# Performance work log

Measured on AMD Instinct MI355X. Metric: run time of the kernel, lower is better.

Reference implementation:

```python
import jax, jax.numpy as jnp
import numpy as np

N = 65536      # total nodes
B = 512        # graphs (equal-sized)
NPER = N // B  # 128 nodes per graph
E = 655360     # edges
F_IN = 128
K = 32         # sort-pool k
OUT = 27


def _gcn(x, row, col, dinv, W, b):
    # PyG GCNConv with added self-loops and symmetric normalization:
    xw = x @ W                                   # [N, F_out]
    coef = dinv[row] * dinv[col]                 # [E]
    agg = jax.ops.segment_sum(xw[row] * coef[:, None], col, num_segments=N)
    return agg + (dinv * dinv)[:, None] * xw + b  # self-loop term + bias


def _conv1d(x, w, b, stride):
    # x: [B, C_in, L], w: [C_out, C_in, K]
    out = jax.lax.conv_general_dilated(x, w, (stride,), 'VALID',
                                       dimension_numbers=('NCH', 'OIH', 'NCH'))
    return out + b[None, :, None]


def setup_inputs() -> dict:
    key = jax.random.key(0)
    ks = jax.random.split(key, 16)
    x = jax.random.normal(ks[0], (N, F_IN), dtype=jnp.float32)
    edge_index = jax.random.randint(ks[1], (2, E), 0, N, dtype=jnp.int32)
    batch = jnp.repeat(jnp.arange(B, dtype=jnp.int32), NPER)

    def lin(k, fi, fo):
        return jax.random.normal(k, (fi, fo), dtype=jnp.float32) / np.sqrt(fi)

    W1, b1 = lin(ks[2], F_IN, 128), jnp.zeros((128,), jnp.float32)
    W2, b2 = lin(ks[3], 128, 64), jnp.zeros((64,), jnp.float32)
    W3, b3 = lin(ks[4], 64, 32), jnp.zeros((32,), jnp.float32)
    W4, b4 = lin(ks[5], 32, 32), jnp.zeros((32,), jnp.float32)
    conv5_w = jax.random.normal(ks[6], (16, 1, 256), jnp.float32) / np.sqrt(256)
    conv5_b = jnp.zeros((16,), jnp.float32)
    conv6_w = jax.random.normal(ks[7], (32, 16, 5), jnp.float32) / np.sqrt(16 * 5)
    conv6_b = jnp.zeros((32,), jnp.float32)
    dense_w = lin(ks[8], 384, OUT)
    dense_b = jnp.zeros((OUT,), jnp.float32)
    return dict(x=x, edge_index=edge_index, batch=batch,
                W1=W1, b1=b1, W2=W2, b2=b2, W3=W3, b3=b3, W4=W4, b4=b4,
                conv5_w=conv5_w, conv5_b=conv5_b, conv6_w=conv6_w, conv6_b=conv6_b,
                dense_w=dense_w, dense_b=dense_b)


def reference(x, edge_index, batch, W1, b1, W2, b2, W3, b3, W4, b4,
              conv5_w, conv5_b, conv6_w, conv6_b, dense_w, dense_b):
    row, col = edge_index[0], edge_index[1]
    deg = jax.ops.segment_sum(jnp.ones((E,), x.dtype), col, num_segments=N) + 1.0
    dinv = jax.lax.rsqrt(deg)

    x1 = jnp.tanh(_gcn(x, row, col, dinv, W1, b1))
    x2 = jnp.tanh(_gcn(x1, row, col, dinv, W2, b2))
    x3 = jnp.tanh(_gcn(x2, row, col, dinv, W3, b3))
    x4 = jnp.tanh(_gcn(x3, row, col, dinv, W4, b4))
    h = jnp.concatenate([x1, x2, x3, x4], axis=-1)   # [N, 256]

    # SortAggregation: sort nodes within each graph by last channel (desc), take top-k.
    hg = h.reshape(B, NPER, 256)
    idx = jnp.argsort(-hg[:, :, -1], axis=1)[:, :K]                 # [B, K]
    pooled = jnp.take_along_axis(hg, idx[:, :, None], axis=1)       # [B, K, 256]
    top_k_indices = idx + (jnp.arange(B, dtype=idx.dtype) * NPER)[:, None]

    z = pooled.reshape(B, 1, K * 256)                # [B, 1, 8192]
    z = jax.nn.relu(_conv1d(z, conv5_w, conv5_b, 256))  # [B, 16, 32]
    z = jax.lax.reduce_window(z, -jnp.inf, jax.lax.max,
                              (1, 1, 2), (1, 1, 2), 'VALID')        # [B, 16, 16]
    z = jax.nn.relu(_conv1d(z, conv6_w, conv6_b, 1))  # [B, 32, 12]
    z = z.reshape(B, -1)                              # [B, 384]
    out = z @ dense_w + dense_b                       # [B, 27]
    return out, top_k_indices
```

## Files before the change

kernel.cpp:

```cpp
#include <hip/hip_runtime.h>
#include <math.h>

#define N_NODES 65536
#define N_EDGES 655360
#define N_GRAPHS 512
#define NPERG 128
#define KTOP 32
#define NOUT 27
#define OUT0_SIZE (N_GRAPHS * NOUT)
#define EPS 64

typedef unsigned int uint32;
typedef unsigned short u16;
typedef unsigned char u8;
typedef __attribute__((ext_vector_type(8))) short bf16x8;
typedef __attribute__((ext_vector_type(4))) float f32x4;
typedef __attribute__((ext_vector_type(2))) float f32x2;

__device__ __forceinline__ float blo(uint32 u) { return __uint_as_float(u << 16); }
__device__ __forceinline__ float bhi(uint32 u) { return __uint_as_float(u & 0xffff0000u); }
__device__ __forceinline__ u16 f2b(float f) {
    uint32 u = __float_as_uint(f);
    u += 0x7fffu + ((u >> 16) & 1u);
    return (u16)(u >> 16);
}
__device__ __forceinline__ uint32 pk(float a, float b) {
    return (uint32)f2b(a) | ((uint32)f2b(b) << 16);
}
__device__ __forceinline__ f32x2 fp8lo(uint32 u) { return __builtin_amdgcn_cvt_pk_f32_fp8((int)u, false); }
__device__ __forceinline__ f32x2 fp8hi(uint32 u) { return __builtin_amdgcn_cvt_pk_f32_fp8((int)u, true); }
__device__ __forceinline__ u8 f2fp8(float v) {
    return (u8)(__builtin_amdgcn_cvt_pk_fp8_f32(v, v, 0, false) & 0xff);
}


template<int FI, int FO>
__device__ __forceinline__ void pack_w(const float* __restrict__ W, uint4* __restrict__ pw,
                                       int base, int nb) {
    constexpr int KC = FI / 8;
    for (int q = (blockIdx.x - base) * 256 + threadIdx.x; q < FO * KC; q += nb * 256) {
        int n = q % FO, c = q / FO;
        const float* wp = W + (size_t)(c * 8) * FO + n;
        uint4 v;
        v.x = pk(wp[0],            wp[(size_t)FO]);
        v.y = pk(wp[2*(size_t)FO], wp[3*(size_t)FO]);
        v.z = pk(wp[4*(size_t)FO], wp[5*(size_t)FO]);
        v.w = pk(wp[6*(size_t)FO], wp[7*(size_t)FO]);
        pw[n * KC + c] = v;
    }
}

__global__ __launch_bounds__(256) void prep_kernel(const float* __restrict__ W1, const float* __restrict__ W2,
                                                   const float* __restrict__ W3, const float* __restrict__ W4,
                                                   uint4* __restrict__ pw1, uint4* __restrict__ pw2,
                                                   uint4* __restrict__ pw3, uint4* __restrict__ pw4,
                                                   int* __restrict__ cur) {
    int b = blockIdx.x;
    if (b < 256) { cur[b * 256 + threadIdx.x] = 0; return; }
    b -= 256;
    if (b < 8)       pack_w<128, 128>(W1, pw1, 256, 8);
    else if (b < 12) pack_w<128, 64>(W2, pw2, 264, 4);
    else if (b < 13) pack_w<64, 32>(W3, pw3, 268, 1);
    else             pack_w<32, 32>(W4, pw4, 269, 1);
}


__global__ __launch_bounds__(256) void fill_kernel(const int* __restrict__ erow, const int* __restrict__ ecol,
                                                   int* __restrict__ cur, u16* __restrict__ ep) {
    int e = blockIdx.x * 256 + threadIdx.x;
    int r = erow[e], d = ecol[e];
    int slot = atomicAdd(&cur[d], 1);
    if (slot < EPS) ep[(d << 6) + slot] = (u16)r;
}


template<int FI, int FO>
__device__ __forceinline__ void stage_Bp(const uint4* __restrict__ pw, uint4* __restrict__ Bs) {
    constexpr int KC = FI / 8, SA = KC + 1;
    for (int q = threadIdx.x; q < FO * KC; q += 256) {
        int n = q / KC, c = q % KC;
        Bs[n * SA + c] = pw[q];
    }
}

template<int FI, int FO, bool OUT_FP8>
__device__ __forceinline__ void mfma_store(uint4* __restrict__ As, const uint4* __restrict__ Bs,
                                           uint4* __restrict__ Y, size_t rowbase,
                                           const float* __restrict__ ds) {
    constexpr int KC = FI / 8, SA = KC + 1;
    constexpr int NTILE = FO / 16;
    constexpr int CW = (NTILE >= 4) ? 4 : NTILE;
    constexpr int NTW = NTILE / CW;
    constexpr int RW = 4 / CW;
    constexpr int RS = 2 / RW;
    constexpr int KSTEPS = FI / 32;
    int t = threadIdx.x;
    int w = t >> 6, L = t & 63;
    int quad = L >> 4, m = L & 15;
    int cw = w % CW, rw = w / CW;

    const bf16x8* Asv = (const bf16x8*)As;
    const bf16x8* Bsv = (const bf16x8*)Bs;

    f32x4 acc[RS][NTW];
#pragma unroll
    for (int i = 0; i < RS; i++)
#pragma unroll
        for (int j = 0; j < NTW; j++) acc[i][j] = (f32x4)0.f;

#pragma unroll
    for (int ks = 0; ks < KSTEPS; ks++) {
        int kc = ks * 4 + quad;
        bf16x8 bfr[NTW];
#pragma unroll
        for (int j = 0; j < NTW; j++) {
            int n = (cw * NTW + j) * 16 + m;
            bfr[j] = Bsv[n * SA + kc];
        }
#pragma unroll
        for (int i = 0; i < RS; i++) {
            int r = (rw * RS + i) * 16 + m;
            bf16x8 afr = Asv[r * SA + kc];
#pragma unroll
            for (int j = 0; j < NTW; j++)
                acc[i][j] = __builtin_amdgcn_mfma_f32_16x16x32_bf16(afr, bfr[j], acc[i][j], 0, 0, 0);
        }
    }
    __syncthreads();

    if constexpr (OUT_FP8) {
        u8* outs = (u8*)As;
#pragma unroll
        for (int i = 0; i < RS; i++) {
            int rb = (rw * RS + i) * 16 + quad * 4;
#pragma unroll
            for (int j = 0; j < NTW; j++) {
                int cc = (cw * NTW + j) * 16 + m;
#pragma unroll
                for (int g2 = 0; g2 < 4; g2++)
                    outs[(rb + g2) * FO + cc] = f2fp8(acc[i][j][g2] * ds[rb + g2]);
            }
        }
    } else {
        u16* outs = (u16*)As;
#pragma unroll
        for (int i = 0; i < RS; i++) {
            int rb = (rw * RS + i) * 16 + quad * 4;
#pragma unroll
            for (int j = 0; j < NTW; j++) {
                int cc = (cw * NTW + j) * 16 + m;
#pragma unroll
                for (int g2 = 0; g2 < 4; g2++)
                    outs[(rb + g2) * FO + cc] = f2b(acc[i][j][g2] * ds[rb + g2]);
            }
        }
    }
    __syncthreads();
    constexpr int NU4 = OUT_FP8 ? (32 * FO / 16) : (32 * FO / 8);
    for (int q = t; q < NU4; q += 256)
        Y[rowbase * (NU4 / 32) + q] = ((const uint4*)As)[q];
}


__global__ __launch_bounds__(256) void gemm1_kernel(const float* __restrict__ x,
                                                    const uint4* __restrict__ pw1,
                                                    const int* __restrict__ cur,
                                                    uint4* __restrict__ xw1) {
    constexpr int KC = 16, SA = 17;
    __shared__ __align__(16) uint4 As[32 * SA];
    __shared__ __align__(16) uint4 Bs[128 * SA];
    __shared__ float ds[32];
    int t = threadIdx.x;
    stage_Bp<128, 128>(pw1, Bs);
    size_t rowbase = (size_t)blockIdx.x * 32;
    if (t < 32) ds[t] = rsqrtf((float)cur[rowbase + t] + 1.0f);
    for (int q = t; q < 32 * KC; q += 256) {
        int r = q / KC, c = q % KC;
        const float* xp = x + (rowbase + r) * 128 + c * 8;
        float4 v0 = *(const float4*)xp;
        float4 v1 = *(const float4*)(xp + 4);
        uint4 u;
        u.x = pk(v0.x, v0.y); u.y = pk(v0.z, v0.w);
        u.z = pk(v1.x, v1.y); u.w = pk(v1.z, v1.w);
        As[r * SA + c] = u;
    }
    __syncthreads();
    mfma_store<128, 128, true>(As, Bs, xw1, rowbase, ds);
}


template<int F>
__device__ __forceinline__ void gath8_fp8v(const uint2* __restrict__ x2, uint4 e8,
                                           int cl, int rem, float (&ac)[8]) {
    constexpr int LN = F / 8;
    uint32 qq[8] = { e8.x & 0xffffu, e8.x >> 16, e8.y & 0xffffu, e8.y >> 16,
                     e8.z & 0xffffu, e8.z >> 16, e8.w & 0xffffu, e8.w >> 16 };
#pragma unroll
    for (int j = 0; j < 8; j++) {
        bool ok = j < rem;
        uint32 src = ok ? qq[j] : 0u;
        uint2 g = x2[(size_t)src * LN + cl];
        uint32 gx = ok ? g.x : 0u, gy = ok ? g.y : 0u;
        f32x2 l0 = fp8lo(gx), h0 = fp8hi(gx), l1 = fp8lo(gy), h1 = fp8hi(gy);
        ac[0] += l0.x; ac[1] += l0.y; ac[2] += h0.x; ac[3] += h0.y;
        ac[4] += l1.x; ac[5] += l1.y; ac[6] += h1.x; ac[7] += h1.y;
    }
}

template<int F>
__device__ __forceinline__ void agg_node_fp8v(const uint2* __restrict__ x2,
                                              const u16* __restrict__ ep,
                                              int n, int cl, int deg, float dn,
                                              const float* __restrict__ bias, float (&r)[8]) {
    constexpr int LN = F / 8;
    const u16* epp = ep + (n << 6);
    float ac[8];
#pragma unroll
    for (int c = 0; c < 8; c++) ac[c] = 0.f;
    uint4 e0 = *(const uint4*)(epp);
    uint4 e1 = *(const uint4*)(epp + 8);
    gath8_fp8v<F>(x2, e0, cl, deg, ac);
    gath8_fp8v<F>(x2, e1, cl, deg - 8, ac);
    if (deg > 16) {
        int nb = min((deg + 7) >> 3, EPS / 8);
        for (int b = 2; b < nb; b++) {
            uint4 e8 = *(const uint4*)(epp + b * 8);
            gath8_fp8v<F>(x2, e8, cl, deg - b * 8, ac);
        }
    }
    uint2 sv = x2[(size_t)n * LN + cl];
    f32x2 l0 = fp8lo(sv.x), h0 = fp8hi(sv.x), l1 = fp8lo(sv.y), h1 = fp8hi(sv.y);
    float sf[8] = { l0.x, l0.y, h0.x, h0.y, l1.x, l1.y, h1.x, h1.y };
#pragma unroll
    for (int c = 0; c < 8; c++) r[c] = dn * (ac[c] + sf[c]) + bias[8 * cl + c];
}


template<int F, int FO, bool OUT_FP8>
__global__ __launch_bounds__(256, 6) void agg_gemm8(const uint2* __restrict__ xin,
                                                    const int* __restrict__ cur,
                                                    const u16* __restrict__ ep,
                                                    const float* __restrict__ bias,
                                                    const uint4* __restrict__ pw,
                                                    uint4* __restrict__ hc4, int co4,
                                                    uint4* __restrict__ xout) {
    constexpr int KC = F / 8, SA = KC + 1;
    constexpr int LN = F / 8;
    constexpr int NPP = 256 / LN;
    __shared__ __align__(16) uint4 As[32 * SA];
    __shared__ __align__(16) uint4 Bs[FO * SA];
    __shared__ float ds[32];
    int t = threadIdx.x;
    int rowbase = blockIdx.x * 32;
    stage_Bp<F, FO>(pw, Bs);
    if (t < 32) ds[t] = rsqrtf((float)cur[rowbase + t] + 1.0f);
    __syncthreads();

    int cl = t % LN, nsub = t / LN;
#pragma unroll
    for (int pass = 0; pass < 32 / NPP; pass++) {
        int nl = pass * NPP + nsub;
        int n = rowbase + nl;
        int deg = cur[n];
        float r[8];
        agg_node_fp8v<F>(xin, ep, n, cl, deg, ds[nl], bias, r);
        uint4 pr;
        pr.x = pk(tanhf(r[0]), tanhf(r[1]));
        pr.y = pk(tanhf(r[2]), tanhf(r[3]));
        pr.z = pk(tanhf(r[4]), tanhf(r[5]));
        pr.w = pk(tanhf(r[6]), tanhf(r[7]));
        hc4[(size_t)n * 32 + co4 + cl] = pr;
        As[nl * SA + cl] = pr;
    }
    __syncthreads();
    mfma_store<F, FO, OUT_FP8>(As, Bs, xout, (size_t)rowbase, ds);
}


template<int L4>
__device__ __forceinline__ void gath8_bf16(const uint2* __restrict__ x2, uint4 e8,
                                           int c4, int rem, float (&ac)[4][4]) {
    uint32 qq[8] = { e8.x & 0xffffu, e8.x >> 16, e8.y & 0xffffu, e8.y >> 16,
                     e8.z & 0xffffu, e8.z >> 16, e8.w & 0xffffu, e8.w >> 16 };
#pragma unroll
    for (int j = 0; j < 8; j++) {
        bool ok = j < rem;
        uint32 src = ok ? qq[j] : 0u;
        uint2 g = x2[(size_t)src * L4 + c4];
        uint32 gx = ok ? g.x : 0u, gy = ok ? g.y : 0u;
        ac[j & 3][0] += blo(gx); ac[j & 3][1] += bhi(gx);
        ac[j & 3][2] += blo(gy); ac[j & 3][3] += bhi(gy);
    }
}

template<int F>
__device__ __forceinline__ void agg_node_bf16(const uint2* __restrict__ x2,
                                              const u16* __restrict__ ep,
                                              int n, int c4, int deg, float dn,
                                              const float* __restrict__ bias,
                                              float& r0, float& r1, float& r2, float& r3) {
    constexpr int L4 = F / 4;
    const u16* epp = ep + (n << 6);
    float ac[4][4];
#pragma unroll
    for (int i = 0; i < 4; i++)
#pragma unroll
        for (int j = 0; j < 4; j++) ac[i][j] = 0.f;
    uint4 e0 = *(const uint4*)(epp);
    uint4 e1 = *(const uint4*)(epp + 8);
    gath8_bf16<L4>(x2, e0, c4, deg, ac);
    gath8_bf16<L4>(x2, e1, c4, deg - 8, ac);
    if (deg > 16) {
        int nb = min((deg + 7) >> 3, EPS / 8);
        for (int b = 2; b < nb; b++) {
            uint4 e8 = *(const uint4*)(epp + b * 8);
            gath8_bf16<L4>(x2, e8, c4, deg - b * 8, ac);
        }
    }
    float s0 = (ac[0][0] + ac[1][0]) + (ac[2][0] + ac[3][0]);
    float s1 = (ac[0][1] + ac[1][1]) + (ac[2][1] + ac[3][1]);
    float s2 = (ac[0][2] + ac[1][2]) + (ac[2][2] + ac[3][2]);
    float s3 = (ac[0][3] + ac[1][3]) + (ac[2][3] + ac[3][3]);
    uint2 sv = x2[(size_t)n * L4 + c4];
    r0 = dn * (s0 + blo(sv.x)) + bias[4 * c4 + 0];
    r1 = dn * (s1 + bhi(sv.x)) + bias[4 * c4 + 1];
    r2 = dn * (s2 + blo(sv.y)) + bias[4 * c4 + 2];
    r3 = dn * (s3 + bhi(sv.y)) + bias[4 * c4 + 3];
}


template<int F, int FO>
__global__ __launch_bounds__(256, 6) void agg_gemm_bf(const uint32* __restrict__ xin,
                                                      const int* __restrict__ cur,
                                                      const u16* __restrict__ ep,
                                                      const float* __restrict__ bias,
                                                      const uint4* __restrict__ pw,
                                                      uint32* __restrict__ hc, int co2,
                                                      uint4* __restrict__ xout) {
    constexpr int KC = F / 8, SA = KC + 1;
    constexpr int L4 = F / 4;
    constexpr int NPP = 256 / L4;
    __shared__ __align__(16) uint4 As[32 * SA];
    __shared__ __align__(16) uint4 Bs[FO * SA];
    __shared__ float ds[32];
    int t = threadIdx.x;
    int rowbase = blockIdx.x * 32;
    stage_Bp<F, FO>(pw, Bs);
    if (t < 32) ds[t] = rsqrtf((float)cur[rowbase + t] + 1.0f);
    __syncthreads();

    uint2* As2 = (uint2*)As;
    uint2* hc2 = (uint2*)hc;
    int c4 = t % L4;
    int nsub = t / L4;
#pragma unroll
    for (int pass = 0; pass < 32 / NPP; pass++) {
        int nl = pass * NPP + nsub;
        int n = rowbase + nl;
        int deg = cur[n];
        float r0, r1, r2, r3;
        agg_node_bf16<F>((const uint2*)xin, ep, n, c4, deg, ds[nl], bias, r0, r1, r2, r3);
        uint2 pr;
        pr.x = pk(tanhf(r0), tanhf(r1));
        pr.y = pk(tanhf(r2), tanhf(r3));
        hc2[(size_t)n * 64 + co2 + c4] = pr;
        As2[nl * (SA * 2) + c4] = pr;
    }
    __syncthreads();
    mfma_store<F, FO, false>(As, Bs, xout, (size_t)rowbase, ds);
}


__device__ __forceinline__ void key_g8(const uint32* __restrict__ xw, uint4 e8,
                                       int rem, float (&ac3)[4]) {
    uint32 qq[8] = { e8.x & 0xffffu, e8.x >> 16, e8.y & 0xffffu, e8.y >> 16,
                     e8.z & 0xffffu, e8.z >> 16, e8.w & 0xffffu, e8.w >> 16 };
#pragma unroll
    for (int j = 0; j < 8; j++) {
        bool ok = j < rem;
        uint32 src = ok ? qq[j] : 0u;
        uint32 gy = xw[(size_t)src * 16 + 15];
        ac3[j & 3] += bhi(ok ? gy : 0u);
    }
}

__global__ __launch_bounds__(256) void final_kernel(const uint32* __restrict__ hc,
                                                    const uint32* __restrict__ xw4,
                                                    const int* __restrict__ cur,
                                                    const u16* __restrict__ ep,
                                                    const float* __restrict__ b4,
                                                    const float* __restrict__ w5, const float* __restrict__ b5,
                                                    const float* __restrict__ w6, const float* __restrict__ b6,
                                                    const float* __restrict__ dw, const float* __restrict__ db,
                                                    float* __restrict__ out) {
    __shared__ float skey[128];
    __shared__ int   sidx[128];
    __shared__ uint32 ph[32 * 133];
    __shared__ __align__(16) float w5s[4096];
    __shared__ float z5[16 * 33];
    __shared__ float ms[16 * 17];
    __shared__ float z6[384];
    int g = blockIdx.x, t = threadIdx.x;

    if (t >= 128) {
        for (int q = t - 128; q < 1024; q += 128)
            ((float4*)w5s)[q] = ((const float4*)w5)[q];
    } else {
        int n = g * NPERG + t;
        int deg = cur[n];
        float dn = rsqrtf((float)deg + 1.0f);
        const u16* epp = ep + (n << 6);
        float ac3[4] = { 0.f, 0.f, 0.f, 0.f };
        uint4 e0 = *(const uint4*)(epp);
        uint4 e1 = *(const uint4*)(epp + 8);
        key_g8(xw4, e0, deg, ac3);
        key_g8(xw4, e1, deg - 8, ac3);
        if (deg > 16) {
            int nb = min((deg + 7) >> 3, EPS / 8);
            for (int b = 2; b < nb; b++) {
                uint4 e8 = *(const uint4*)(epp + b * 8);
                key_g8(xw4, e8, deg - b * 8, ac3);
            }
        }
        float s3 = (ac3[0] + ac3[1]) + (ac3[2] + ac3[3]);
        uint32 svy = xw4[(size_t)n * 16 + 15];
        float r3 = dn * (s3 + bhi(svy)) + b4[31];
        skey[t] = __uint_as_float(((uint32)f2b(tanhf(r3))) << 16);
        sidx[t] = t;
    }
    __syncthreads();

    for (int sz = 2; sz <= 128; sz <<= 1) {
        for (int stride = sz >> 1; stride > 0; stride >>= 1) {
            if (t < 64) {
                int i = ((t & ~(stride - 1)) << 1) | (t & (stride - 1));
                int j = i | stride;
                float ki = skey[i], kj = skey[j];
                int ii = sidx[i], ij = sidx[j];
                bool desc = ((i & sz) == 0);
                bool ibef = (ki > kj) || (ki == kj && ii < ij);
                if (desc != ibef) { skey[i] = kj; skey[j] = ki; sidx[i] = ij; sidx[j] = ii; }
            }
            __syncthreads();
        }
    }

    if (t < KTOP) out[OUT0_SIZE + g * KTOP + t] = (float)(g * NPERG + sidx[t]);

    {
        int r = t >> 3, c4 = t & 7;
        int n = g * NPERG + sidx[r];
        int deg = cur[n];
        float dn = rsqrtf((float)deg + 1.0f);
        float r0, r1, r2, r3;
        agg_node_bf16<32>((const uint2*)xw4, ep, n, c4, deg, dn, b4, r0, r1, r2, r3);
        uint32* dst = &ph[r * 133 + 112 + 2 * c4];
        dst[0] = pk(tanhf(r0), tanhf(r1));
        dst[1] = pk(tanhf(r2), tanhf(r3));
    }

    {
        const uint4* hcv = (const uint4*)hc;
        for (int q = t; q < 1024; q += 256) {
            int cell = q & 31;
            if (cell >= 28) continue;
            int r2 = q >> 5;
            int node = g * NPERG + sidx[r2];
            uint4 v = hcv[(size_t)node * 32 + cell];
            uint32* dst = &ph[r2 * 133 + cell * 4];
            dst[0] = v.x; dst[1] = v.y; dst[2] = v.z; dst[3] = v.w;
        }
    }
    __syncthreads();

    {
        int o = t >> 5, l = t & 31;
        float a0 = 0.f, a1 = 0.f;
#pragma unroll 4
        for (int j2 = 0; j2 < 128; j2++) {
            uint32 u = ph[l * 133 + j2];
            float p0 = blo(u), p1 = bhi(u);
            a0 += p0 * w5s[o * 256 + 2 * j2]       + p1 * w5s[o * 256 + 2 * j2 + 1];
            a1 += p0 * w5s[(o + 8) * 256 + 2 * j2] + p1 * w5s[(o + 8) * 256 + 2 * j2 + 1];
        }
        z5[o * 33 + l]       = fmaxf(a0 + b5[o], 0.f);
        z5[(o + 8) * 33 + l] = fmaxf(a1 + b5[o + 8], 0.f);
    }
    __syncthreads();

    {
        int o = t >> 4, p = t & 15;
        ms[o * 17 + p] = fmaxf(z5[o * 33 + 2 * p], z5[o * 33 + 2 * p + 1]);
    }
    __syncthreads();

    for (int q = t; q < 384; q += 256) {
        int o2 = q / 12, tt = q % 12;
        float a = b6[o2];
        for (int o = 0; o < 16; o++) {
#pragma unroll
            for (int k = 0; k < 5; k++)
                a += w6[(o2 * 16 + o) * 5 + k] * ms[o * 17 + tt + k];
        }
        z6[q] = fmaxf(a, 0.f);
    }
    __syncthreads();

    if (t < NOUT) {
        float a = db[t];
        for (int i = 0; i < 384; i++) a += z6[i] * dw[i * NOUT + t];
        out[g * NOUT + t] = a;
    }
}


extern "C" void kernel_launch(void* const* d_in, const int* in_sizes, int n_in,
                              void* d_out, int out_size, void* d_ws, size_t ws_size,
                              hipStream_t stream) {
    const float* x    = (const float*)d_in[0];
    const int*   edge = (const int*)d_in[1];
    const int*   erow = edge;
    const int*   ecol = edge + N_EDGES;
    const float* W1 = (const float*)d_in[3];  const float* b1 = (const float*)d_in[4];
    const float* W2 = (const float*)d_in[5];  const float* b2 = (const float*)d_in[6];
    const float* W3 = (const float*)d_in[7];  const float* b3 = (const float*)d_in[8];
    const float* W4 = (const float*)d_in[9];  const float* b4 = (const float*)d_in[10];
    const float* w5 = (const float*)d_in[11]; const float* b5 = (const float*)d_in[12];
    const float* w6 = (const float*)d_in[13]; const float* b6 = (const float*)d_in[14];
    const float* dw = (const float*)d_in[15]; const float* db = (const float*)d_in[16];
    float* out = (float*)d_out;

    char* wsb = (char*)d_ws;
    size_t off = 0;
    auto alloc = [&](size_t bytes) -> void* {
        void* p = wsb + off;
        off = (off + bytes + 255) & ~(size_t)255;
        return p;
    };
    int*    cur  = (int*)   alloc((size_t)N_NODES * 4);
    u16*    ep   = (u16*)   alloc((size_t)N_NODES * EPS * 2);
    uint32* xwA  = (uint32*)alloc((size_t)N_NODES * 32 * 4);
    uint32* xwB  = (uint32*)alloc((size_t)N_NODES * 32 * 4);
    uint32* hc   = (uint32*)alloc((size_t)N_NODES * 128 * 4);
    uint4*  pw1  = (uint4*) alloc(2048 * 16);
    uint4*  pw2  = (uint4*) alloc(1024 * 16);
    uint4*  pw3  = (uint4*) alloc(256 * 16);
    uint4*  pw4  = (uint4*) alloc(128 * 16);
    (void)ws_size; (void)in_sizes; (void)n_in; (void)out_size;

    prep_kernel<<<270, 256, 0, stream>>>(W1, W2, W3, W4, pw1, pw2, pw3, pw4, cur);
    fill_kernel<<<N_EDGES / 256, 256, 0, stream>>>(erow, ecol, cur, ep);
    gemm1_kernel<<<N_NODES / 32, 256, 0, stream>>>(x, pw1, cur, (uint4*)xwA);
    agg_gemm8<128, 64, true><<<N_NODES / 32, 256, 0, stream>>>((const uint2*)xwA, cur, ep, b1, pw2, (uint4*)hc, 0, (uint4*)xwB);
    agg_gemm8<64, 32, false><<<N_NODES / 32, 256, 0, stream>>>((const uint2*)xwB, cur, ep, b2, pw3, (uint4*)hc, 16, (uint4*)xwA);
    agg_gemm_bf<32, 32><<<N_NODES / 32, 256, 0, stream>>>(xwA, cur, ep, b3, pw4, hc, 48, (uint4*)xwB);
    final_kernel<<<N_GRAPHS, 256, 0, stream>>>(hc, xwB, cur, ep, b4, w5, b5, w6, b6, dw, db, out);
}
```

Before: 226.1 us.

## Widen layer-1 gathers, batch first 16 neighbor loads, add nontemporal stores

Adds a new agg_gemm16 kernel for layer 1 in which each thread gathers 16 fp8 channels (uint4) per neighbor and handles one node, instead of 8 channels over several passes. The fp8 and bf16 aggregation helpers now issue all 16 neighbor loads before accumulating, to raise memory-level parallelism. Edge index and x reads and the concatenated-feature stores switch to nontemporal loads and stores to limit cache pollution. The changes cost more registers per thread, which could lower occupancy.

```diff
diff --git a/kernel.cpp b/kernel.cpp
--- a/kernel.cpp
+++ b/kernel.cpp
@@ -16,6 +16,9 @@
 typedef __attribute__((ext_vector_type(8))) short bf16x8;
 typedef __attribute__((ext_vector_type(4))) float f32x4;
 typedef __attribute__((ext_vector_type(2))) float f32x2;
+typedef __attribute__((ext_vector_type(4))) float f32x4n;
+typedef __attribute__((ext_vector_type(4))) uint32 u32x4;
+typedef __attribute__((ext_vector_type(2))) uint32 u32x2;
 
 __device__ __forceinline__ float blo(uint32 u) { return __uint_as_float(u << 16); }
 __device__ __forceinline__ float bhi(uint32 u) { return __uint_as_float(u & 0xffff0000u); }
@@ -31,6 +34,15 @@
 __device__ __forceinline__ f32x2 fp8hi(uint32 u) { return __builtin_amdgcn_cvt_pk_f32_fp8((int)u, true); }
 __device__ __forceinline__ u8 f2fp8(float v) {
     return (u8)(__builtin_amdgcn_cvt_pk_fp8_f32(v, v, 0, false) & 0xff);
+}
+
+__device__ __forceinline__ void nts4(uint4* p, uint4 v) {
+    u32x4 vv; vv.x = v.x; vv.y = v.y; vv.z = v.z; vv.w = v.w;
+    __builtin_nontemporal_store(vv, (u32x4*)p);
+}
+__device__ __forceinline__ void nts2(uint2* p, uint2 v) {
+    u32x2 vv; vv.x = v.x; vv.y = v.y;
+    __builtin_nontemporal_store(vv, (u32x2*)p);
 }
 
 
@@ -68,7 +80,8 @@
 __global__ __launch_bounds__(256) void fill_kernel(const int* __restrict__ erow, const int* __restrict__ ecol,
                                                    int* __restrict__ cur, u16* __restrict__ ep) {
     int e = blockIdx.x * 256 + threadIdx.x;
-    int r = erow[e], d = ecol[e];
+    int r = __builtin_nontemporal_load(erow + e);
+    int d = __builtin_nontemporal_load(ecol + e);
     int slot = atomicAdd(&cur[d], 1);
     if (slot < EPS) ep[(d << 6) + slot] = (u16)r;
 }
@@ -176,9 +189,9 @@
     if (t < 32) ds[t] = rsqrtf((float)cur[rowbase + t] + 1.0f);
     for (int q = t; q < 32 * KC; q += 256) {
         int r = q / KC, c = q % KC;
-        const float* xp = x + (rowbase + r) * 128 + c * 8;
-        float4 v0 = *(const float4*)xp;
-        float4 v1 = *(const float4*)(xp + 4);
+        const f32x4n* xp4 = (const f32x4n*)(x + (rowbase + r) * 128 + c * 8);
+        f32x4n v0 = __builtin_nontemporal_load(xp4);
+        f32x4n v1 = __builtin_nontemporal_load(xp4 + 1);
         uint4 u;
         u.x = pk(v0.x, v0.y); u.y = pk(v0.z, v0.w);
         u.z = pk(v1.x, v1.y); u.w = pk(v1.z, v1.w);
@@ -186,6 +199,96 @@
     }
     __syncthreads();
     mfma_store<128, 128, true>(As, Bs, xw1, rowbase, ds);
+}
+
+
+__device__ __forceinline__ void gath8_fp8w(const uint4* __restrict__ x4, uint4 e8,
+                                           int cl, int rem, float (&ac)[16]) {
+    uint32 qq[8] = { e8.x & 0xffffu, e8.x >> 16, e8.y & 0xffffu, e8.y >> 16,
+                     e8.z & 0xffffu, e8.z >> 16, e8.w & 0xffffu, e8.w >> 16 };
+#pragma unroll
+    for (int j = 0; j < 8; j++) {
+        bool ok = j < rem;
+        uint32 src = ok ? qq[j] : 0u;
+        uint4 g = x4[(size_t)src * 8 + cl];
+        uint32 gw0 = ok ? g.x : 0u, gw1 = ok ? g.y : 0u;
+        uint32 gw2 = ok ? g.z : 0u, gw3 = ok ? g.w : 0u;
+        f32x2 a0 = fp8lo(gw0), b0 = fp8hi(gw0), a1 = fp8lo(gw1), b1 = fp8hi(gw1);
+        f32x2 a2 = fp8lo(gw2), b2 = fp8hi(gw2), a3 = fp8lo(gw3), b3 = fp8hi(gw3);
+        ac[0] += a0.x;  ac[1] += a0.y;  ac[2] += b0.x;  ac[3] += b0.y;
+        ac[4] += a1.x;  ac[5] += a1.y;  ac[6] += b1.x;  ac[7] += b1.y;
+        ac[8] += a2.x;  ac[9] += a2.y;  ac[10] += b2.x; ac[11] += b2.y;
+        ac[12] += a3.x; ac[13] += a3.y; ac[14] += b3.x; ac[15] += b3.y;
+    }
+}
+
+__device__ __forceinline__ void agg_node_fp8w(const uint4* __restrict__ x4,
+                                              const u16* __restrict__ ep,
+                                              int n, int cl, int deg, float dn,
+                                              const float* __restrict__ bias, float (&r)[16]) {
+    const u16* epp = ep + (n << 6);
+    float ac[16];
+#pragma unroll
+    for (int c = 0; c < 16; c++) ac[c] = 0.f;
+    uint4 e0 = *(const uint4*)(epp);
+    uint4 e1 = *(const uint4*)(epp + 8);
+    gath8_fp8w(x4, e0, cl, deg, ac);
+    gath8_fp8w(x4, e1, cl, deg - 8, ac);
+    if (deg > 16) {
+        int nb = min((deg + 7) >> 3, EPS / 8);
+        for (int b = 2; b < nb; b++) {
+            uint4 e8 = *(const uint4*)(epp + b * 8);
+            gath8_fp8w(x4, e8, cl, deg - b * 8, ac);
+        }
+    }
+    uint4 sv = x4[(size_t)n * 8 + cl];
+    f32x2 a0 = fp8lo(sv.x), b0 = fp8hi(sv.x), a1 = fp8lo(sv.y), b1 = fp8hi(sv.y);
+    f32x2 a2 = fp8lo(sv.z), b2 = fp8hi(sv.z), a3 = fp8lo(sv.w), b3 = fp8hi(sv.w);
+    float sf[16] = { a0.x, a0.y, b0.x, b0.y, a1.x, a1.y, b1.x, b1.y,
+                     a2.x, a2.y, b2.x, b2.y, a3.x, a3.y, b3.x, b3.y };
+#pragma unroll
+    for (int c = 0; c < 16; c++) r[c] = dn * (ac[c] + sf[c]) + bias[16 * cl + c];
+}
+
+
+template<int FO>
+__global__ __launch_bounds__(256, 6) void agg_gemm16(const uint4* __restrict__ xin,
+                                                     const int* __restrict__ cur,
+                                                     const u16* __restrict__ ep,
+                                                     const float* __restrict__ bias,
+                                                     const uint4* __restrict__ pw,
+                                                     uint4* __restrict__ hc4, int co4,
+                                                     uint4* __restrict__ xout) {
+    constexpr int KC = 16, SA = 17;
+    __shared__ __align__(16) uint4 As[32 * SA];
+    __shared__ __align__(16) uint4 Bs[FO * SA];
+    __shared__ float ds[32];
+    int t = threadIdx.x;
+    int rowbase = blockIdx.x * 32;
+    stage_Bp<128, FO>(pw, Bs);
+    if (t < 32) ds[t] = rsqrtf((float)cur[rowbase + t] + 1.0f);
+    __syncthreads();
+
+    int cl = t & 7, nl = t >> 3;
+    int n = rowbase + nl;
+    int deg = cur[n];
+    float r[16];
+    agg_node_fp8w(xin, ep, n, cl, deg, ds[nl], bias, r);
+    uint4 pr0, pr1;
+    pr0.x = pk(tanhf(r[0]),  tanhf(r[1]));
+    pr0.y = pk(tanhf(r[2]),  tanhf(r[3]));
+    pr0.z = pk(tanhf(r[4]),  tanhf(r[5]));
+    pr0.w = pk(tanhf(r[6]),  tanhf(r[7]));
+    pr1.x = pk(tanhf(r[8]),  tanhf(r[9]));
+    pr1.y = pk(tanhf(r[10]), tanhf(r[11]));
+    pr1.z = pk(tanhf(r[12]), tanhf(r[13]));
+    pr1.w = pk(tanhf(r[14]), tanhf(r[15]));
+    nts4(&hc4[(size_t)n * 32 + co4 + 2 * cl], pr0);
+    nts4(&hc4[(size_t)n * 32 + co4 + 2 * cl + 1], pr1);
+    As[nl * SA + 2 * cl]     = pr0;
+    As[nl * SA + 2 * cl + 1] = pr1;
+    __syncthreads();
+    mfma_store<128, FO, true>(As, Bs, xout, (size_t)rowbase, ds);
 }
 
 
@@ -214,13 +317,29 @@
                                               const float* __restrict__ bias, float (&r)[8]) {
     constexpr int LN = F / 8;
     const u16* epp = ep + (n << 6);
-    float ac[8];
-#pragma unroll
-    for (int c = 0; c < 8; c++) ac[c] = 0.f;
     uint4 e0 = *(const uint4*)(epp);
     uint4 e1 = *(const uint4*)(epp + 8);
-    gath8_fp8v<F>(x2, e0, cl, deg, ac);
-    gath8_fp8v<F>(x2, e1, cl, deg - 8, ac);
+    uint32 qq[16] = { e0.x & 0xffffu, e0.x >> 16, e0.y & 0xffffu, e0.y >> 16,
+                      e0.z & 0xffffu, e0.z >> 16, e0.w & 0xffffu, e0.w >> 16,
+                      e1.x & 0xffffu, e1.x >> 16, e1.y & 0xffffu, e1.y >> 16,
+                      e1.z & 0xffffu, e1.z >> 16, e1.w & 0xffffu, e1.w >> 16 };
+    uint2 g[16];
+#pragma unroll
+    for (int j = 0; j < 16; j++) {
+        uint32 src = (j < deg) ? qq[j] : 0u;
+        g[j] = x2[(size_t)src * LN + cl];
+    }
+    float ac[8];
+#pragma unroll
+    for (int c = 0; c < 8; c++) ac[c] = 0.f;
+#pragma unroll
+    for (int j = 0; j < 16; j++) {
+        bool ok = j < deg;
+        uint32 gx = ok ? g[j].x : 0u, gy = ok ? g[j].y : 0u;
+        f32x2 l0 = fp8lo(gx), h0 = fp8hi(gx), l1 = fp8lo(gy), h1 = fp8hi(gy);
+        ac[0] += l0.x; ac[1] += l0.y; ac[2] += h0.x; ac[3] += h0.y;
+        ac[4] += l1.x; ac[5] += l1.y; ac[6] += h1.x; ac[7] += h1.y;
+    }
     if (deg > 16) {
         int nb = min((deg + 7) >> 3, EPS / 8);
         for (int b = 2; b < nb; b++) {
@@ -269,7 +388,7 @@
         pr.y = pk(tanhf(r[2]), tanhf(r[3]));
         pr.z = pk(tanhf(r[4]), tanhf(r[5]));
         pr.w = pk(tanhf(r[6]), tanhf(r[7]));
-        hc4[(size_t)n * 32 + co4 + cl] = pr;
+        nts4(&hc4[(size_t)n * 32 + co4 + cl], pr);
         As[nl * SA + cl] = pr;
     }
     __syncthreads();
@@ -301,15 +420,30 @@
                                               float& r0, float& r1, float& r2, float& r3) {
     constexpr int L4 = F / 4;
     const u16* epp = ep + (n << 6);
-    float ac[4][4];
-#pragma unroll
-    for (int i = 0; i < 4; i++)
-#pragma unroll
-        for (int j = 0; j < 4; j++) ac[i][j] = 0.f;
     uint4 e0 = *(const uint4*)(epp);
     uint4 e1 = *(const uint4*)(epp + 8);
-    gath8_bf16<L4>(x2, e0, c4, deg, ac);
-    gath8_bf16<L4>(x2, e1, c4, deg - 8, ac);
+    uint32 qq[16] = { e0.x & 0xffffu, e0.x >> 16, e0.y & 0xffffu, e0.y >> 16,
+                      e0.z & 0xffffu, e0.z >> 16, e0.w & 0xffffu, e0.w >> 16,
+                      e1.x & 0xffffu, e1.x >> 16, e1.y & 0xffffu, e1.y >> 16,
+                      e1.z & 0xffffu, e1.z >> 16, e1.w & 0xffffu, e1.w >> 16 };
+    uint2 g[16];
+#pragma unroll
+    for (int j = 0; j < 16; j++) {
+        uint32 src = (j < deg) ? qq[j] : 0u;
+        g[j] = x2[(size_t)src * L4 + c4];
+    }
+    float ac[4][4];
+#pragma unroll
+    for (int i = 0; i < 4; i++)
+#pragma unroll
+        for (int j = 0; j < 4; j++) ac[i][j] = 0.f;
+#pragma unroll
+    for (int j = 0; j < 16; j++) {
+        bool ok = j < deg;
+        uint32 gx = ok ? g[j].x : 0u, gy = ok ? g[j].y : 0u;
+        ac[j & 3][0] += blo(gx); ac[j & 3][1] += bhi(gx);
+        ac[j & 3][2] += blo(gy); ac[j & 3][3] += bhi(gy);
+    }
     if (deg > 16) {
         int nb = min((deg + 7) >> 3, EPS / 8);
         for (int b = 2; b < nb; b++) {
@@ -363,7 +497,7 @@
         uint2 pr;
         pr.x = pk(tanhf(r0), tanhf(r1));
         pr.y = pk(tanhf(r2), tanhf(r3));
-        hc2[(size_t)n * 64 + co2 + c4] = pr;
+        nts2(&hc2[(size_t)n * 64 + co2 + c4], pr);
         As2[nl * (SA * 2) + c4] = pr;
     }
     __syncthreads();
@@ -551,7 +685,7 @@
     prep_kernel<<<270, 256, 0, stream>>>(W1, W2, W3, W4, pw1, pw2, pw3, pw4, cur);
     fill_kernel<<<N_EDGES / 256, 256, 0, stream>>>(erow, ecol, cur, ep);
     gemm1_kernel<<<N_NODES / 32, 256, 0, stream>>>(x, pw1, cur, (uint4*)xwA);
-    agg_gemm8<128, 64, true><<<N_NODES / 32, 256, 0, stream>>>((const uint2*)xwA, cur, ep, b1, pw2, (uint4*)hc, 0, (uint4*)xwB);
+    agg_gemm16<64><<<N_NODES / 32, 256, 0, stream>>>((const uint4*)xwA, cur, ep, b1, pw2, (uint4*)hc, 0, (uint4*)xwB);
     agg_gemm8<64, 32, false><<<N_NODES / 32, 256, 0, stream>>>((const uint2*)xwB, cur, ep, b2, pw3, (uint4*)hc, 16, (uint4*)xwA);
     agg_gemm_bf<32, 32><<<N_NODES / 32, 256, 0, stream>>>(xwA, cur, ep, b3, pw4, hc, 48, (uint4*)xwB);
     final_kernel<<<N_GRAPHS, 256, 0, stream>>>(hc, xwB, cur, ep, b4, w5, b5, w6, b6, dw, db, out);
```

New measurement: 239.0 us. 5.7% more time.
